# Performance work log

Hardware: AMD Instinct MI355X
Metric: run time of the kernel (lower is better)

The kernel has to match this reference:

```python
import jax, jax.numpy as jnp
import numpy as np

B, S, D, H, KD = 4, 2048, 640, 10, 64


def setup_inputs() -> dict:
    key = jax.random.key(0)
    k0, k1, k2, k3, k4 = jax.random.split(key, 5)
    x = jax.random.normal(k0, (B, S, D), dtype=jnp.float32)
    # per-head projection weights, stacked over heads: [H, D, KD]
    Wq = jax.random.normal(k1, (H, D, KD), dtype=jnp.float32) * 0.05
    Wk = jax.random.normal(k2, (H, D, KD), dtype=jnp.float32) * 0.05
    Wv = jax.random.normal(k3, (H, D, KD), dtype=jnp.float32) * 0.05
    # output projection: [H*KD, D]
    Wo = jax.random.normal(k4, (H * KD, D), dtype=jnp.float32) * 0.05
    return {"x": x, "Wq": Wq, "Wk": Wk, "Wv": Wv, "Wo": Wo}


def reference(x, Wq, Wk, Wv, Wo):
    # Batched equivalent of the per-head Python loop:
    # each head computes q=x@Wq_h, k=x@Wk_h, v=x@Wv_h, softmax(q k^T / sqrt(KD)) @ v
    q = jnp.einsum("bsd,hdk->bhsk", x, Wq)
    k = jnp.einsum("bsd,hdk->bhsk", x, Wk)
    v = jnp.einsum("bsd,hdk->bhsk", x, Wv)
    scale = 1.0 / jnp.sqrt(jnp.asarray(KD, x.dtype))
    scores = jnp.einsum("bhsk,bhtk->bhst", q, k) * scale  # [B,H,S,S]
    attn = jax.nn.softmax(scores, axis=-1)
    z = jnp.einsum("bhst,bhtk->bhsk", attn, v)  # [B,H,S,KD]
    # concat heads along last axis (head 0 first, matching the loop order)
    z = z.transpose(0, 2, 1, 3).reshape(x.shape[0], x.shape[1], H * KD)
    return jnp.einsum("bsf,fd->bsd", z, Wo)
```

## Files before the change

kernel.cpp:

```cpp
#include <hip/hip_runtime.h>
#include <hip/hip_bf16.h>

#define B_  4
#define S_  2048
#define D_  640
#define H_  10
#define KD_ 64

typedef __attribute__((ext_vector_type(8))) short  short8;
typedef __attribute__((ext_vector_type(4))) short  short4v;
typedef __attribute__((ext_vector_type(4))) float  floatx4;
typedef __attribute__((ext_vector_type(2))) unsigned int uint2v;

static __device__ __forceinline__ short f2bf_fast(float f) {
    unsigned int u = __float_as_uint(f);
    u += 0x7fffu + ((u >> 16) & 1u);
    return (short)(u >> 16);
}
static __device__ __forceinline__ unsigned int pack2bf(float a, float b) {
    unsigned int ua = __float_as_uint(a), ub = __float_as_uint(b);
    ua += 0x7fffu + ((ua >> 16) & 1u);
    ub += 0x7fffu + ((ub >> 16) & 1u);
    return (ua >> 16) | (ub & 0xffff0000u);
}

static __device__ __forceinline__ void gload_lds16(const void* gp, void* lp) {
    __builtin_amdgcn_global_load_lds(
        (const __attribute__((address_space(1))) unsigned int*)gp,
        (__attribute__((address_space(3))) unsigned int*)lp, 16, 0, 0);
}

__global__ __launch_bounds__(256) void prep(
        const float* __restrict__ x,
        const float* __restrict__ Wq, const float* __restrict__ Wk,
        const float* __restrict__ Wv, const float* __restrict__ Wo,
        short* __restrict__ xb, short* __restrict__ BigT,
        short* __restrict__ WoT) {
    __shared__ float tile[32][33];
    int bid = blockIdx.x;
    if (bid < 5120) {
        int idx = (bid * 256 + threadIdx.x) * 4;
        float4 v = *(const float4*)(x + idx);
        uint2v o;
        o[0] = pack2bf(v.x, v.y);
        o[1] = pack2bf(v.z, v.w);
        *(uint2v*)(xb + idx) = o;
    } else if (bid < 6320) {
        int flat = bid - 5120;
        int bz = flat / 40, rem = flat % 40;
        int by = rem >> 1, bxx = rem & 1;
        int w = bz / 10, h = bz % 10;
        const float* W = ((w == 0) ? Wq : (w == 1) ? Wk : Wv) + h * 640 * 64;
        short* out = BigT + (w * 640 + h * 64) * 640;
        int c0 = bxx * 32;
        int r0 = by * 32;
        int tx = threadIdx.x & 31, ty = threadIdx.x >> 5;
        #pragma unroll
        for (int k = 0; k < 4; ++k)
            tile[ty + 8 * k][tx] = W[(r0 + ty + 8 * k) * 64 + c0 + tx];
        __syncthreads();
        #pragma unroll
        for (int k = 0; k < 4; ++k)
            out[(c0 + ty + 8 * k) * 640 + r0 + tx] = f2bf_fast(tile[tx][ty + 8 * k]);
    } else {
        int flat = bid - 6320;
        int c0 = (flat % 20) * 32;
        int r0 = (flat / 20) * 32;
        int tx = threadIdx.x & 31, ty = threadIdx.x >> 5;
        #pragma unroll
        for (int k = 0; k < 4; ++k)
            tile[ty + 8 * k][tx] = Wo[(r0 + ty + 8 * k) * 640 + c0 + tx];
        __syncthreads();
        #pragma unroll
        for (int k = 0; k < 4; ++k)
            WoT[(c0 + ty + 8 * k) * 640 + r0 + tx] = f2bf_fast(tile[tx][ty + 8 * k]);
    }
}

__global__ __launch_bounds__(256) void qkv_gemm(
        const short* __restrict__ X, const short* __restrict__ BigT,
        short* __restrict__ qb, short* __restrict__ kb, short* __restrict__ vtb) {
    __shared__ __align__(16) short Ab[128][64];
    __shared__ __align__(16) short Bb[128][64];

    int wave = threadIdx.x >> 6;
    int lane = threadIdx.x & 63;
    int lq = lane & 15, quad = lane >> 4;
    int wm = (wave & 1) * 64, wn = (wave >> 1) * 64;
    int tm = blockIdx.x * 128;
    int tn = blockIdx.y * 128;

    int r8 = lane >> 3;
    int sc = ((lane & 7) ^ r8) * 8;
    const short* Asrc = X    + (tm + wave * 32 + r8) * 640 + sc;
    const short* Bsrc = BigT + (tn + wave * 32 + r8) * 640 + sc;

    floatx4 acc[4][4];
    for (int a = 0; a < 4; ++a)
        for (int n = 0; n < 4; ++n)
            acc[a][n] = (floatx4){0.f, 0.f, 0.f, 0.f};

    int swz = lq & 7;

    if (tn < 1280) {
        for (int k0 = 0; k0 < 640; k0 += 64) {
            __syncthreads();
            #pragma unroll
            for (int c = 0; c < 4; ++c) {
                gload_lds16(Asrc + c * 8 * 640 + k0, &Ab[wave * 32 + c * 8][0]);
                gload_lds16(Bsrc + c * 8 * 640 + k0, &Bb[wave * 32 + c * 8][0]);
            }
            __syncthreads();
            #pragma unroll
            for (int ks = 0; ks < 2; ++ks) {
                short8 af[4], bf[4];
                #pragma unroll
                for (int t = 0; t < 4; ++t) {
                    af[t] = *(const short8*)(&Ab[wm + t * 16 + lq][((ks * 4 + quad) ^ swz) * 8]);
                    bf[t] = *(const short8*)(&Bb[wn + t * 16 + lq][((ks * 4 + quad) ^ swz) * 8]);
                }
                #pragma unroll
                for (int mt = 0; mt < 4; ++mt)
                    #pragma unroll
                    for (int nt = 0; nt < 4; ++nt)
                        acc[mt][nt] = __builtin_amdgcn_mfma_f32_16x16x32_bf16(
                            af[mt], bf[nt], acc[mt][nt], 0, 0, 0);
            }
        }
        const float qscale = 0.18033688011112042f;
        short* dst = (tn < 640) ? qb : kb;
        float scale = (tn < 640) ? qscale : 1.0f;
        #pragma unroll
        for (int nt = 0; nt < 4; ++nt) {
            int rem = (tn + wn + nt * 16) % 640;
            int hh = rem / 64, kd = (rem % 64) + lq;
            #pragma unroll
            for (int mt = 0; mt < 4; ++mt) {
                #pragma unroll
                for (int r = 0; r < 4; ++r) {
                    int m = tm + wm + mt * 16 + quad * 4 + r;
                    int b = m >> 11, s = m & 2047;
                    dst[((b * H_ + hh) * S_ + s) * KD_ + kd] =
                        f2bf_fast(acc[mt][nt][r] * scale);
                }
            }
        }
    } else {
        for (int k0 = 0; k0 < 640; k0 += 64) {
            __syncthreads();
            #pragma unroll
            for (int c = 0; c < 4; ++c) {
                gload_lds16(Asrc + c * 8 * 640 + k0, &Ab[wave * 32 + c * 8][0]);
                gload_lds16(Bsrc + c * 8 * 640 + k0, &Bb[wave * 32 + c * 8][0]);
            }
            __syncthreads();
            #pragma unroll
            for (int ks = 0; ks < 2; ++ks) {
                short8 af[4], bf[4];
                #pragma unroll
                for (int t = 0; t < 4; ++t) {
                    af[t] = *(const short8*)(&Ab[wm + t * 16 + lq][((ks * 4 + quad) ^ swz) * 8]);
                    bf[t] = *(const short8*)(&Bb[wn + t * 16 + lq][((ks * 4 + quad) ^ swz) * 8]);
                }
                #pragma unroll
                for (int nt = 0; nt < 4; ++nt)
                    #pragma unroll
                    for (int mt = 0; mt < 4; ++mt)
                        acc[nt][mt] = __builtin_amdgcn_mfma_f32_16x16x32_bf16(
                            bf[nt], af[mt], acc[nt][mt], 0, 0, 0);
            }
        }
        #pragma unroll
        for (int nt = 0; nt < 4; ++nt) {
            int rem = (tn + wn + nt * 16) - 1280;
            int hh = rem / 64;
            int kd0 = (rem % 64) + quad * 4;
            #pragma unroll
            for (int mt = 0; mt < 4; ++mt) {
                int m = tm + wm + mt * 16 + lq;
                int b = m >> 11, s = m & 2047;
                #pragma unroll
                for (int r = 0; r < 4; ++r) {
                    vtb[((b * H_ + hh) * KD_ + kd0 + r) * S_ + s] =
                        f2bf_fast(acc[nt][mt][r]);
                }
            }
        }
    }
}

__global__ __launch_bounds__(256, 3) void attn(
        const short* __restrict__ qb, const short* __restrict__ kbuf,
        const short* __restrict__ vtb, short* __restrict__ zb) {
    __shared__ __align__(16) short Kbuf[2][64][64];
    __shared__ __align__(16) short Vbuf[2][64][64];
    __shared__ __align__(16) short Pbuf[4][2][16][72];

    int wave = threadIdx.x >> 6;
    int lane = threadIdx.x & 63;
    int lq = lane & 15, quad = lane >> 4;

    int bx = blockIdx.x;
    int xcd = bx & 7, slot = bx >> 3;
    int bh = xcd * 5 + (slot >> 4);
    int qt = slot & 15;
    int b = bh / 10, h = bh % 10;
    int q0 = qt * 128;

    const short* qp = qb + (b * H_ + h) * S_ * KD_;
    const short* kp = kbuf + (b * H_ + h) * S_ * KD_;
    const short* vp = vtb + (b * H_ + h) * KD_ * S_;

    int r8 = lane >> 3;
    int g  = (lane & 7) ^ r8;
    const short* kg0 = kp + (wave * 16 + r8) * 64 + g * 8;
    const short* kg1 = kp + (wave * 16 + 8 + r8) * 64 + g * 8;
    const short* vg0 = vp + (wave * 16 + r8) * (long)S_ + g * 8;
    const short* vg1 = vp + (wave * 16 + 8 + r8) * (long)S_ + g * 8;

    short8 qA0, qA1, qB0, qB1;
    {
        int rowA = q0 + wave * 32 + lq;
        qA0 = *(const short8*)(qp + rowA * 64 + quad * 8);
        qA1 = *(const short8*)(qp + rowA * 64 + 32 + quad * 8);
        qB0 = *(const short8*)(qp + (rowA + 16) * 64 + quad * 8);
        qB1 = *(const short8*)(qp + (rowA + 16) * 64 + 32 + quad * 8);
    }

    short8 ones;
    #pragma unroll
    for (int i = 0; i < 8; ++i) ones[i] = (short)0x3F80;

    floatx4 OA[4], OB[4];
    for (int n = 0; n < 4; ++n) {
        OA[n] = (floatx4){0.f, 0.f, 0.f, 0.f};
        OB[n] = (floatx4){0.f, 0.f, 0.f, 0.f};
    }
    floatx4 lsvA = (floatx4){0.f, 0.f, 0.f, 0.f};
    floatx4 lsvB = (floatx4){0.f, 0.f, 0.f, 0.f};

    gload_lds16(kg0, &Kbuf[0][wave * 16][0]);
    gload_lds16(kg1, &Kbuf[0][wave * 16 + 8][0]);
    gload_lds16(vg0, &Vbuf[0][wave * 16][0]);
    gload_lds16(vg1, &Vbuf[0][wave * 16 + 8][0]);

    int p = 0;
    int sw = lq & 7;

    for (int t0 = 0; t0 < S_; t0 += 64) {
        __syncthreads();

        if (t0 + 64 < S_) {
            int pn = p ^ 1;
            gload_lds16(kg0 + (t0 + 64) * 64, &Kbuf[pn][wave * 16][0]);
            gload_lds16(kg1 + (t0 + 64) * 64, &Kbuf[pn][wave * 16 + 8][0]);
            gload_lds16(vg0 + (t0 + 64),      &Vbuf[pn][wave * 16][0]);
            gload_lds16(vg1 + (t0 + 64),      &Vbuf[pn][wave * 16 + 8][0]);
        }

        const short* Kb = &Kbuf[p][0][0];
        const short* Vb = &Vbuf[p][0][0];

        floatx4 sTA[4], sTB[4];
        #pragma unroll
        for (int kblk = 0; kblk < 4; ++kblk) {
            const short* krow = Kb + (kblk * 16 + lq) * 64;
            short8 bk0 = *(const short8*)(krow + (quad ^ sw) * 8);
            short8 bk1 = *(const short8*)(krow + ((quad + 4) ^ sw) * 8);
            floatx4 zA = (floatx4){0.f, 0.f, 0.f, 0.f};
            zA = __builtin_amdgcn_mfma_f32_16x16x32_bf16(bk0, qA0, zA, 0, 0, 0);
            sTA[kblk] = __builtin_amdgcn_mfma_f32_16x16x32_bf16(bk1, qA1, zA, 0, 0, 0);
            floatx4 zB = (floatx4){0.f, 0.f, 0.f, 0.f};
            zB = __builtin_amdgcn_mfma_f32_16x16x32_bf16(bk0, qB0, zB, 0, 0, 0);
            sTB[kblk] = __builtin_amdgcn_mfma_f32_16x16x32_bf16(bk1, qB1, zB, 0, 0, 0);
        }

        #pragma unroll
        for (int kblk = 0; kblk < 4; ++kblk) {
            uint2v wa;
            wa[0] = pack2bf(__builtin_amdgcn_exp2f(sTA[kblk][0]),
                            __builtin_amdgcn_exp2f(sTA[kblk][1]));
            wa[1] = pack2bf(__builtin_amdgcn_exp2f(sTA[kblk][2]),
                            __builtin_amdgcn_exp2f(sTA[kblk][3]));
            *(uint2v*)(&Pbuf[wave][0][lq][kblk * 16 + quad * 4]) = wa;
            uint2v wb;
            wb[0] = pack2bf(__builtin_amdgcn_exp2f(sTB[kblk][0]),
                            __builtin_amdgcn_exp2f(sTB[kblk][1]));
            wb[1] = pack2bf(__builtin_amdgcn_exp2f(sTB[kblk][2]),
                            __builtin_amdgcn_exp2f(sTB[kblk][3]));
            *(uint2v*)(&Pbuf[wave][1][lq][kblk * 16 + quad * 4]) = wb;
        }

        #pragma unroll
        for (int ts = 0; ts < 2; ++ts) {
            short8 pfA = *(const short8*)(&Pbuf[wave][0][lq][ts * 32 + quad * 8]);
            short8 pfB = *(const short8*)(&Pbuf[wave][1][lq][ts * 32 + quad * 8]);
            lsvA = __builtin_amdgcn_mfma_f32_16x16x32_bf16(ones, pfA, lsvA, 0, 0, 0);
            lsvB = __builtin_amdgcn_mfma_f32_16x16x32_bf16(ones, pfB, lsvB, 0, 0, 0);
            #pragma unroll
            for (int db = 0; db < 4; ++db) {
                const short* vrow = Vb + (db * 16 + lq) * 64;
                short8 bv = *(const short8*)(vrow + ((ts * 4 + quad) ^ sw) * 8);
                OA[db] = __builtin_amdgcn_mfma_f32_16x16x32_bf16(bv, pfA, OA[db], 0, 0, 0);
                OB[db] = __builtin_amdgcn_mfma_f32_16x16x32_bf16(bv, pfB, OB[db], 0, 0, 0);
            }
        }

        p ^= 1;
    }

    float invA = 1.0f / lsvA[0];
    float invB = 1.0f / lsvB[0];

    int sA = q0 + wave * 32 + lq;
    int sB = sA + 16;
    short* zrA = zb + (b * S_ + sA) * 640 + h * 64;
    short* zrB = zb + (b * S_ + sB) * 640 + h * 64;
    #pragma unroll
    for (int db = 0; db < 4; ++db) {
        uint2v za, zv;
        za[0] = pack2bf(OA[db][0] * invA, OA[db][1] * invA);
        za[1] = pack2bf(OA[db][2] * invA, OA[db][3] * invA);
        *(uint2v*)(zrA + db * 16 + quad * 4) = za;
        zv[0] = pack2bf(OB[db][0] * invB, OB[db][1] * invB);
        zv[1] = pack2bf(OB[db][2] * invB, OB[db][3] * invB);
        *(uint2v*)(zrB + db * 16 + quad * 4) = zv;
    }
}

__global__ __launch_bounds__(256) void out_gemm(
        const short* __restrict__ Z, const short* __restrict__ WoT,
        float* __restrict__ out) {
    __shared__ __align__(16) short Ab[128][64];
    __shared__ __align__(16) short Bb[128][64];

    int wave = threadIdx.x >> 6;
    int lane = threadIdx.x & 63;
    int lq = lane & 15, quad = lane >> 4;
    int wm = (wave & 1) * 64, wn = (wave >> 1) * 64;
    int tm = blockIdx.x * 128;
    int tn = blockIdx.y * 128;

    int r8 = lane >> 3;
    int sc = ((lane & 7) ^ r8) * 8;
    const short* Asrc = Z   + (tm + wave * 32 + r8) * 640 + sc;
    const short* Bsrc = WoT + (tn + wave * 32 + r8) * 640 + sc;

    floatx4 acc[4][4];
    for (int a = 0; a < 4; ++a)
        for (int n = 0; n < 4; ++n)
            acc[a][n] = (floatx4){0.f, 0.f, 0.f, 0.f};

    int swz = lq & 7;
    for (int k0 = 0; k0 < 640; k0 += 64) {
        __syncthreads();
        #pragma unroll
        for (int c = 0; c < 4; ++c) {
            gload_lds16(Asrc + c * 8 * 640 + k0, &Ab[wave * 32 + c * 8][0]);
            gload_lds16(Bsrc + c * 8 * 640 + k0, &Bb[wave * 32 + c * 8][0]);
        }
        __syncthreads();

        #pragma unroll
        for (int ks = 0; ks < 2; ++ks) {
            short8 af[4], bf[4];
            #pragma unroll
            for (int t = 0; t < 4; ++t) {
                af[t] = *(const short8*)(&Ab[wm + t * 16 + lq][((ks * 4 + quad) ^ swz) * 8]);
                bf[t] = *(const short8*)(&Bb[wn + t * 16 + lq][((ks * 4 + quad) ^ swz) * 8]);
            }
            #pragma unroll
            for (int mt = 0; mt < 4; ++mt)
                #pragma unroll
                for (int nt = 0; nt < 4; ++nt)
                    acc[mt][nt] = __builtin_amdgcn_mfma_f32_16x16x32_bf16(
                        af[mt], bf[nt], acc[mt][nt], 0, 0, 0);
        }
    }

    #pragma unroll
    for (int mt = 0; mt < 4; ++mt) {
        #pragma unroll
        for (int nt = 0; nt < 4; ++nt) {
            #pragma unroll
            for (int r = 0; r < 4; ++r) {
                int m = tm + wm + mt * 16 + quad * 4 + r;
                out[m * 640 + tn + wn + nt * 16 + lq] = acc[mt][nt][r];
            }
        }
    }
}

extern "C" void kernel_launch(void* const* d_in, const int* in_sizes, int n_in,
                              void* d_out, int out_size, void* d_ws, size_t ws_size,
                              hipStream_t stream) {
    const float* x  = (const float*)d_in[0];
    const float* Wq = (const float*)d_in[1];
    const float* Wk = (const float*)d_in[2];
    const float* Wv = (const float*)d_in[3];
    const float* Wo = (const float*)d_in[4];
    float* out = (float*)d_out;

    char* ws = (char*)d_ws;
    short* BigT = (short*)(ws);
    short* WoT  = (short*)(ws + 2457600);
    short* xb   = (short*)(ws + 3276800);
    short* qb   = (short*)(ws + 13762560);
    short* kb   = (short*)(ws + 24248320);
    short* vtb  = (short*)(ws + 34734080);
    short* zb   = (short*)(ws + 45219840);

    prep<<<dim3(6720), dim3(256), 0, stream>>>(x, Wq, Wk, Wv, Wo, xb, BigT, WoT);
    qkv_gemm<<<dim3(64, 15), dim3(256), 0, stream>>>(xb, BigT, qb, kb, vtb);
    attn<<<dim3(640), dim3(256), 0, stream>>>(qb, kb, vtb, zb);
    out_gemm<<<dim3(64, 5), dim3(256), 0, stream>>>(zb, WoT, out);
}
```

Measured before the change: 190.4 us.

## Double-buffer LDS tiles with K-step 32 in QKV and output GEMMs

Both projection GEMMs switch from a single 128x64 LDS tile with two barriers per K step to two 128x32 buffers. The next K slice is prefetched with global_load_lds while the current one feeds the MFMAs, so only one barrier is needed per step. The XOR swizzle is redone for the 32-wide rows, and the duplicated V/QK loops are merged into one loop that branches on the MFMA operand order. The bf16 pair packing now uses the HIP __float22bfloat162_rn intrinsic. The trade-off is twice as many loop iterations and barriers at a smaller K step, with overlap limited to one step.

```diff
diff --git a/kernel.cpp b/kernel.cpp
--- a/kernel.cpp
+++ b/kernel.cpp
@@ -18,10 +18,9 @@
     return (short)(u >> 16);
 }
 static __device__ __forceinline__ unsigned int pack2bf(float a, float b) {
-    unsigned int ua = __float_as_uint(a), ub = __float_as_uint(b);
-    ua += 0x7fffu + ((ua >> 16) & 1u);
-    ub += 0x7fffu + ((ub >> 16) & 1u);
-    return (ua >> 16) | (ub & 0xffff0000u);
+    union { __hip_bfloat162 h; unsigned int u; } c;
+    c.h = __float22bfloat162_rn(float2{a, b});
+    return c.u;
 }
 
 static __device__ __forceinline__ void gload_lds16(const void* gp, void* lp) {
@@ -77,11 +76,12 @@
     }
 }
 
+
 __global__ __launch_bounds__(256) void qkv_gemm(
         const short* __restrict__ X, const short* __restrict__ BigT,
         short* __restrict__ qb, short* __restrict__ kb, short* __restrict__ vtb) {
-    __shared__ __align__(16) short Ab[128][64];
-    __shared__ __align__(16) short Bb[128][64];
+    __shared__ __align__(16) short Ab[2][128][32];
+    __shared__ __align__(16) short Bb[2][128][32];
 
     int wave = threadIdx.x >> 6;
     int lane = threadIdx.x & 63;
@@ -90,43 +90,63 @@
     int tm = blockIdx.x * 128;
     int tn = blockIdx.y * 128;
 
-    int r8 = lane >> 3;
-    int sc = ((lane & 7) ^ r8) * 8;
-    const short* Asrc = X    + (tm + wave * 32 + r8) * 640 + sc;
-    const short* Bsrc = BigT + (tn + wave * 32 + r8) * 640 + sc;
+    int srow = lane >> 2;
+    int schunk = (lane & 3) ^ ((lane >> 3) & 3);
+    const short* Asrc0 = X    + (tm + wave * 32 + srow) * 640 + schunk * 8;
+    const short* Bsrc0 = BigT + (tn + wave * 32 + srow) * 640 + schunk * 8;
+    const short* Asrc1 = Asrc0 + 16 * 640;
+    const short* Bsrc1 = Bsrc0 + 16 * 640;
 
     floatx4 acc[4][4];
     for (int a = 0; a < 4; ++a)
         for (int n = 0; n < 4; ++n)
             acc[a][n] = (floatx4){0.f, 0.f, 0.f, 0.f};
 
-    int swz = lq & 7;
-
-    if (tn < 1280) {
-        for (int k0 = 0; k0 < 640; k0 += 64) {
-            __syncthreads();
-            #pragma unroll
-            for (int c = 0; c < 4; ++c) {
-                gload_lds16(Asrc + c * 8 * 640 + k0, &Ab[wave * 32 + c * 8][0]);
-                gload_lds16(Bsrc + c * 8 * 640 + k0, &Bb[wave * 32 + c * 8][0]);
-            }
-            __syncthreads();
-            #pragma unroll
-            for (int ks = 0; ks < 2; ++ks) {
-                short8 af[4], bf[4];
+    int rsw = (lq >> 1) & 3;
+
+    gload_lds16(Asrc0, &Ab[0][wave * 32][0]);
+    gload_lds16(Asrc1, &Ab[0][wave * 32 + 16][0]);
+    gload_lds16(Bsrc0, &Bb[0][wave * 32][0]);
+    gload_lds16(Bsrc1, &Bb[0][wave * 32 + 16][0]);
+
+    int p = 0;
+    bool isV = (tn >= 1280);
+
+    for (int k0 = 0; k0 < 640; k0 += 32) {
+        __syncthreads();
+        if (k0 + 32 < 640) {
+            int pn = p ^ 1;
+            gload_lds16(Asrc0 + k0 + 32, &Ab[pn][wave * 32][0]);
+            gload_lds16(Asrc1 + k0 + 32, &Ab[pn][wave * 32 + 16][0]);
+            gload_lds16(Bsrc0 + k0 + 32, &Bb[pn][wave * 32][0]);
+            gload_lds16(Bsrc1 + k0 + 32, &Bb[pn][wave * 32 + 16][0]);
+        }
+
+        short8 af[4], bf[4];
+        #pragma unroll
+        for (int t = 0; t < 4; ++t) {
+            af[t] = *(const short8*)(&Ab[p][wm + t * 16 + lq][(quad ^ rsw) * 8]);
+            bf[t] = *(const short8*)(&Bb[p][wn + t * 16 + lq][(quad ^ rsw) * 8]);
+        }
+        if (!isV) {
+            #pragma unroll
+            for (int mt = 0; mt < 4; ++mt)
                 #pragma unroll
-                for (int t = 0; t < 4; ++t) {
-                    af[t] = *(const short8*)(&Ab[wm + t * 16 + lq][((ks * 4 + quad) ^ swz) * 8]);
-                    bf[t] = *(const short8*)(&Bb[wn + t * 16 + lq][((ks * 4 + quad) ^ swz) * 8]);
-                }
+                for (int nt = 0; nt < 4; ++nt)
+                    acc[mt][nt] = __builtin_amdgcn_mfma_f32_16x16x32_bf16(
+                        af[mt], bf[nt], acc[mt][nt], 0, 0, 0);
+        } else {
+            #pragma unroll
+            for (int nt = 0; nt < 4; ++nt)
                 #pragma unroll
                 for (int mt = 0; mt < 4; ++mt)
-                    #pragma unroll
-                    for (int nt = 0; nt < 4; ++nt)
-                        acc[mt][nt] = __builtin_amdgcn_mfma_f32_16x16x32_bf16(
-                            af[mt], bf[nt], acc[mt][nt], 0, 0, 0);
-            }
-        }
+                    acc[nt][mt] = __builtin_amdgcn_mfma_f32_16x16x32_bf16(
+                        bf[nt], af[mt], acc[nt][mt], 0, 0, 0);
+        }
+        p ^= 1;
+    }
+
+    if (!isV) {
         const float qscale = 0.18033688011112042f;
         short* dst = (tn < 640) ? qb : kb;
         float scale = (tn < 640) ? qscale : 1.0f;
@@ -146,30 +166,6 @@
             }
         }
     } else {
-        for (int k0 = 0; k0 < 640; k0 += 64) {
-            __syncthreads();
-            #pragma unroll
-            for (int c = 0; c < 4; ++c) {
-                gload_lds16(Asrc + c * 8 * 640 + k0, &Ab[wave * 32 + c * 8][0]);
-                gload_lds16(Bsrc + c * 8 * 640 + k0, &Bb[wave * 32 + c * 8][0]);
-            }
-            __syncthreads();
-            #pragma unroll
-            for (int ks = 0; ks < 2; ++ks) {
-                short8 af[4], bf[4];
-                #pragma unroll
-                for (int t = 0; t < 4; ++t) {
-                    af[t] = *(const short8*)(&Ab[wm + t * 16 + lq][((ks * 4 + quad) ^ swz) * 8]);
-                    bf[t] = *(const short8*)(&Bb[wn + t * 16 + lq][((ks * 4 + quad) ^ swz) * 8]);
-                }
-                #pragma unroll
-                for (int nt = 0; nt < 4; ++nt)
-                    #pragma unroll
-                    for (int mt = 0; mt < 4; ++mt)
-                        acc[nt][mt] = __builtin_amdgcn_mfma_f32_16x16x32_bf16(
-                            bf[nt], af[mt], acc[nt][mt], 0, 0, 0);
-            }
-        }
         #pragma unroll
         for (int nt = 0; nt < 4; ++nt) {
             int rem = (tn + wn + nt * 16) - 1280;
@@ -331,8 +327,8 @@
 __global__ __launch_bounds__(256) void out_gemm(
         const short* __restrict__ Z, const short* __restrict__ WoT,
         float* __restrict__ out) {
-    __shared__ __align__(16) short Ab[128][64];
-    __shared__ __align__(16) short Bb[128][64];
+    __shared__ __align__(16) short Ab[2][128][32];
+    __shared__ __align__(16) short Bb[2][128][32];
 
     int wave = threadIdx.x >> 6;
     int lane = threadIdx.x & 63;
@@ -341,41 +337,49 @@
     int tm = blockIdx.x * 128;
     int tn = blockIdx.y * 128;
 
-    int r8 = lane >> 3;
-    int sc = ((lane & 7) ^ r8) * 8;
-    const short* Asrc = Z   + (tm + wave * 32 + r8) * 640 + sc;
-    const short* Bsrc = WoT + (tn + wave * 32 + r8) * 640 + sc;
+    int srow = lane >> 2;
+    int schunk = (lane & 3) ^ ((lane >> 3) & 3);
+    const short* Asrc0 = Z   + (tm + wave * 32 + srow) * 640 + schunk * 8;
+    const short* Bsrc0 = WoT + (tn + wave * 32 + srow) * 640 + schunk * 8;
+    const short* Asrc1 = Asrc0 + 16 * 640;
+    const short* Bsrc1 = Bsrc0 + 16 * 640;
 
     floatx4 acc[4][4];
     for (int a = 0; a < 4; ++a)
         for (int n = 0; n < 4; ++n)
             acc[a][n] = (floatx4){0.f, 0.f, 0.f, 0.f};
 
-    int swz = lq & 7;
-    for (int k0 = 0; k0 < 640; k0 += 64) {
+    int rsw = (lq >> 1) & 3;
+
+    gload_lds16(Asrc0, &Ab[0][wave * 32][0]);
+    gload_lds16(Asrc1, &Ab[0][wave * 32 + 16][0]);
+    gload_lds16(Bsrc0, &Bb[0][wave * 32][0]);
+    gload_lds16(Bsrc1, &Bb[0][wave * 32 + 16][0]);
+
+    int p = 0;
+    for (int k0 = 0; k0 < 640; k0 += 32) {
         __syncthreads();
-        #pragma unroll
-        for (int c = 0; c < 4; ++c) {
-            gload_lds16(Asrc + c * 8 * 640 + k0, &Ab[wave * 32 + c * 8][0]);
-            gload_lds16(Bsrc + c * 8 * 640 + k0, &Bb[wave * 32 + c * 8][0]);
-        }
-        __syncthreads();
-
-        #pragma unroll
-        for (int ks = 0; ks < 2; ++ks) {
-            short8 af[4], bf[4];
-            #pragma unroll
-            for (int t = 0; t < 4; ++t) {
-                af[t] = *(const short8*)(&Ab[wm + t * 16 + lq][((ks * 4 + quad) ^ swz) * 8]);
-                bf[t] = *(const short8*)(&Bb[wn + t * 16 + lq][((ks * 4 + quad) ^ swz) * 8]);
-            }
-            #pragma unroll
-            for (int mt = 0; mt < 4; ++mt)
-                #pragma unroll
-                for (int nt = 0; nt < 4; ++nt)
-                    acc[mt][nt] = __builtin_amdgcn_mfma_f32_16x16x32_bf16(
-                        af[mt], bf[nt], acc[mt][nt], 0, 0, 0);
-        }
+        if (k0 + 32 < 640) {
+            int pn = p ^ 1;
+            gload_lds16(Asrc0 + k0 + 32, &Ab[pn][wave * 32][0]);
+            gload_lds16(Asrc1 + k0 + 32, &Ab[pn][wave * 32 + 16][0]);
+            gload_lds16(Bsrc0 + k0 + 32, &Bb[pn][wave * 32][0]);
+            gload_lds16(Bsrc1 + k0 + 32, &Bb[pn][wave * 32 + 16][0]);
+        }
+
+        short8 af[4], bf[4];
+        #pragma unroll
+        for (int t = 0; t < 4; ++t) {
+            af[t] = *(const short8*)(&Ab[p][wm + t * 16 + lq][(quad ^ rsw) * 8]);
+            bf[t] = *(const short8*)(&Bb[p][wn + t * 16 + lq][(quad ^ rsw) * 8]);
+        }
+        #pragma unroll
+        for (int mt = 0; mt < 4; ++mt)
+            #pragma unroll
+            for (int nt = 0; nt < 4; ++nt)
+                acc[mt][nt] = __builtin_amdgcn_mfma_f32_16x16x32_bf16(
+                    af[mt], bf[nt], acc[mt][nt], 0, 0, 0);
+        p ^= 1;
     }
 
     #pragma unroll
```

Result: no change. 190.2 us (-0.1%).
